# Optimization experiments

Measured on AMD Instinct MI355X. Metric: run time of the kernel, lower is better.

The kernel has to match this reference:

```python
import jax, jax.numpy as jnp
import numpy as np

HSV_BINS = 32
LBP_BINS = 256
NEG_SLOPE = 0.2
ENV_CLASSES = 4
SEASON_CLASSES = 4


def rgb_to_hsv(img):
    # img: [N, 3, H, W] in [0, 1]
    img = jnp.clip(img, 0.0, 1.0)
    r, g, b = img[:, 0], img[:, 1], img[:, 2]
    maxc = img.max(axis=1)
    minc = img.min(axis=1)
    delta = maxc - minc
    mask = delta > 1e-6
    safe = jnp.where(mask, delta, 1.0)
    hue = jnp.zeros_like(maxc)
    hue = jnp.where((maxc == r) & mask, jnp.mod((g - b) / safe, 6.0), hue)
    hue = jnp.where((maxc == g) & mask, (b - r) / safe + 2.0, hue)
    hue = jnp.where((maxc == b) & mask, (r - g) / safe + 4.0, hue)
    hue = hue / 6.0
    sat = jnp.where(maxc > 1e-6, delta / jnp.maximum(maxc, 1e-6), jnp.zeros_like(maxc))
    return jnp.stack((hue, sat, maxc), axis=1)


def hist_features(hsv):
    # torch.histc(bins=32, min=0, max=1); HSV values are all in [0,1],
    # value==1.0 falls into the last bin -> clip(floor(v*bins), 0, bins-1).
    N, C, H, W = hsv.shape
    v = hsv.reshape(N * C, H * W)
    idx = jnp.clip(jnp.floor(v * HSV_BINS).astype(jnp.int32), 0, HSV_BINS - 1)
    offset = jnp.arange(N * C, dtype=jnp.int32)[:, None] * HSV_BINS
    counts = jnp.bincount((idx + offset).reshape(-1), length=N * C * HSV_BINS)
    counts = counts.reshape(N * C, HSV_BINS).astype(jnp.float32)
    counts = counts / jnp.maximum(counts.sum(-1, keepdims=True), 1.0)
    return counts.reshape(N, C * HSV_BINS)


def lbp_features(hsv):
    N, C, H, W = hsv.shape
    p = jnp.pad(hsv, ((0, 0), (0, 0), (1, 1), (1, 1)), mode='reflect')
    offsets = [(0, 0), (0, 1), (0, 2), (1, 2), (2, 2), (2, 1), (2, 0), (1, 0)]
    codes = jnp.zeros((N, C, H, W), dtype=jnp.int32)
    for bit, (dy, dx) in enumerate(offsets):
        nb = jax.lax.dynamic_slice(p, (0, 0, dy, dx), (N, C, H, W))
        codes = codes + (nb >= hsv).astype(jnp.int32) * (1 << bit)
    codes = codes.reshape(N * C, H * W)
    offset = jnp.arange(N * C, dtype=jnp.int32)[:, None] * LBP_BINS
    counts = jnp.bincount((codes + offset).reshape(-1), length=N * C * LBP_BINS)
    counts = counts.reshape(N * C, LBP_BINS).astype(jnp.float32)
    counts = counts / jnp.maximum(counts.sum(-1, keepdims=True), 1.0)
    return counts.reshape(N, C * LBP_BINS)


def setup_inputs() -> dict:
    key = jax.random.key(0)
    k1, k2, k3, k4, k5 = jax.random.split(key, 5)
    B, T, H, W = 4, 8, 512, 512
    sequence = jax.random.uniform(k1, (B, T, 3, H, W), dtype=jnp.float32)
    high = jax.random.normal(k2, (B * T, 2048), dtype=jnp.float32)
    Wp = jax.random.normal(k3, (512, 2912), dtype=jnp.float32) * 0.02
    bp = jnp.zeros((512,), dtype=jnp.float32)
    environment_id = jax.random.randint(k4, (B,), 0, ENV_CLASSES, dtype=jnp.int64 if jax.config.jax_enable_x64 else jnp.int32)
    season_id = jax.random.randint(k5, (B,), 0, SEASON_CLASSES, dtype=jnp.int64 if jax.config.jax_enable_x64 else jnp.int32)
    return {"sequence": sequence, "high": high, "W": Wp, "b": bp,
            "environment_id": environment_id, "season_id": season_id}


def reference(sequence, high, W, b, environment_id, season_id):
    B, T, C, H, Wd = sequence.shape
    # inputs are already in [0,1) so _to_unit_rgb reduces to a clamp
    frames = jnp.clip(sequence, 0.0, 1.0).reshape(B * T, C, H, Wd)
    hsv = rgb_to_hsv(frames)                                   # [BT,3,H,W]
    low = jnp.concatenate((hist_features(hsv), lbp_features(hsv)), axis=1)  # [BT,864]
    fused = jnp.concatenate((high, low), axis=1).reshape(B, T, -1)          # [B,T,2912]
    aggregated = fused.mean(axis=1)                             # [B,2912]
    z = aggregated @ W.T + b                                    # Linear(2912->512)
    c_feat = jnp.where(z >= 0, z, NEG_SLOPE * z)                # LeakyReLU(0.2)
    env = jax.nn.one_hot(environment_id, ENV_CLASSES, dtype=jnp.float32)
    season = jax.nn.one_hot(season_id, SEASON_CLASSES, dtype=jnp.float32)
    c_cls = jnp.concatenate((env, season), axis=1)
    return (c_feat, c_cls)
```

## Files before the change

kernel.cpp:

```cpp
#include <hip/hip_runtime.h>

#define IMH 512
#define IMW 512
#define NFRAMES 32
#define HSV_BINS 32
#define LBP_BINS 256
#define FEAT_HIGH 2048
#define FEAT_LOW (3*HSV_BINS + 3*LBP_BINS)
#define FEAT_TOT (FEAT_HIGH + FEAT_LOW)
#define OUT_COLS 512
#define RSTRIP 16
#define STRIPS (IMH / RSTRIP)
#define HALVES 2
#define NHREP 16
#define NLREP 4

__device__ __forceinline__ void rgb2hsv(float r, float g, float b,
                                        float& h, float& s, float& v) {
    float maxc = fmaxf(r, fmaxf(g, b));
    float minc = fminf(r, fminf(g, b));
    float delta = maxc - minc;
    bool mask = delta > 1e-6f;
    float rd = __builtin_amdgcn_rcpf(mask ? delta : 1.0f);
    float hue = 0.0f;
    if (mask) {
        if (maxc == r) { float t = (g - b) * rd; hue = (t >= 0.0f) ? t : t + 6.0f; }
        if (maxc == g) hue = (b - r) * rd + 2.0f;
        if (maxc == b) hue = (r - g) * rd + 4.0f;
    }
    h = hue * (1.0f / 6.0f);
    s = (maxc > 1e-6f) ? delta * __builtin_amdgcn_rcpf(maxc) : 0.0f;
    v = maxc;
}

struct Row { float hl, hc, hr, sl, sc, sr, vl, vc, vr; };

__device__ __forceinline__ void cvt_shfl(const float* __restrict__ pR,
                                         const float* __restrict__ pG,
                                         const float* __restrict__ pB,
                                         int ry, int x, int lane,
                                         float r, float g, float b, Row& o) {
    rgb2hsv(r, g, b, o.hc, o.sc, o.vc);
    o.hl = __shfl(o.hc, (lane + 63) & 63);
    o.sl = __shfl(o.sc, (lane + 63) & 63);
    o.vl = __shfl(o.vc, (lane + 63) & 63);
    o.hr = __shfl(o.hc, (lane + 1) & 63);
    o.sr = __shfl(o.sc, (lane + 1) & 63);
    o.vr = __shfl(o.vc, (lane + 1) & 63);
    if (lane == 0 || lane == 63) {
        int xe = (lane == 0) ? x - 1 : x + 1;
        if (xe < 0) xe = 1;
        if (xe > IMW - 1) xe = IMW - 2;
        size_t eo = (size_t)ry * IMW + xe;
        float he, se, ve;
        rgb2hsv(pR[eo], pG[eo], pB[eo], he, se, ve);
        if (lane == 0) { o.hl = he; o.sl = se; o.vl = ve; }
        else           { o.hr = he; o.sr = se; o.vr = ve; }
    }
}

__device__ __forceinline__ void emit1(float ul, float uc, float ur,
                                      float cl, float ce, float cr,
                                      float dl, float dc, float dr,
                                      unsigned* __restrict__ hb,
                                      unsigned* __restrict__ lb) {
    int code = 0;
    code |= (ul >= ce) ? 1   : 0;
    code |= (uc >= ce) ? 2   : 0;
    code |= (ur >= ce) ? 4   : 0;
    code |= (cr >= ce) ? 8   : 0;
    code |= (dr >= ce) ? 16  : 0;
    code |= (dc >= ce) ? 32  : 0;
    code |= (dl >= ce) ? 64  : 0;
    code |= (cl >= ce) ? 128 : 0;
    int bin = min((int)(ce * 32.0f), HSV_BINS - 1);
    atomicAdd(hb + bin, 1u);
    atomicAdd(lb + code, 1u);
}

__global__ __launch_bounds__(256, 4) void hist_lbp_kernel(const float* __restrict__ seq,
                                                          unsigned* __restrict__ hist_g,
                                                          unsigned* __restrict__ lbp_g) {
    const int bid   = blockIdx.x;
    const int n     = bid >> 6;
    const int rem   = bid & 63;
    const int strip = rem >> 1;
    const int half  = rem & 1;
    const int tid   = threadIdx.x;
    const int lane  = tid & 63;
    const int w     = tid >> 6;
    const int x     = half * 256 + w * 64 + lane;
    const int yb    = strip * RSTRIP;

    __shared__ unsigned sh_hist[3][NHREP][HSV_BINS + 1];
    __shared__ unsigned sh_lbp[3][NLREP][LBP_BINS + 1];

    for (int i = tid; i < 3 * NHREP * (HSV_BINS + 1); i += 256) ((unsigned*)sh_hist)[i] = 0u;
    for (int i = tid; i < 3 * NLREP * (LBP_BINS + 1); i += 256) ((unsigned*)sh_lbp)[i] = 0u;
    __syncthreads();

    unsigned* hb0 = &sh_hist[0][lane & (NHREP - 1)][0];
    unsigned* hb1 = &sh_hist[1][lane & (NHREP - 1)][0];
    unsigned* hb2 = &sh_hist[2][lane & (NHREP - 1)][0];
    unsigned* lb0 = &sh_lbp[0][lane & (NLREP - 1)][0];
    unsigned* lb1 = &sh_lbp[1][lane & (NLREP - 1)][0];
    unsigned* lb2 = &sh_lbp[2][lane & (NLREP - 1)][0];

    const float* pR = seq + (size_t)n * 3 * IMH * IMW;
    const float* pG = pR + (size_t)IMH * IMW;
    const float* pB = pR + 2 * (size_t)IMH * IMW;

    Row U, C, D;
    const int ytop = (yb == 0) ? 1 : yb - 1;
    {
        size_t o = (size_t)ytop * IMW + x;
        cvt_shfl(pR, pG, pB, ytop, x, lane, pR[o], pG[o], pB[o], U);
        o = (size_t)yb * IMW + x;
        cvt_shfl(pR, pG, pB, yb, x, lane, pR[o], pG[o], pB[o], C);
    }
    float rn, gn, bn;
    {
        size_t o = (size_t)(yb + 1) * IMW + x;
        rn = pR[o]; gn = pG[o]; bn = pB[o];
    }

#pragma unroll 2
    for (int i = 0; i < RSTRIP; ++i) {
        int ry = yb + 1 + i;
        if (ry == IMH) ry = IMH - 2;
        cvt_shfl(pR, pG, pB, ry, x, lane, rn, gn, bn, D);
        if (i < RSTRIP - 1) {
            int r2 = yb + 2 + i;
            if (r2 == IMH) r2 = IMH - 2;
            size_t o = (size_t)r2 * IMW + x;
            rn = pR[o]; gn = pG[o]; bn = pB[o];
        }
        emit1(U.hl, U.hc, U.hr, C.hl, C.hc, C.hr, D.hl, D.hc, D.hr, hb0, lb0);
        emit1(U.sl, U.sc, U.sr, C.sl, C.sc, C.sr, D.sl, D.sc, D.sr, hb1, lb1);
        emit1(U.vl, U.vc, U.vr, C.vl, C.vc, C.vr, D.vl, D.vc, D.vr, hb2, lb2);
        U = C; C = D;
    }

    __syncthreads();
    for (int i = tid; i < 3 * HSV_BINS; i += 256) {
        int c = i >> 5, b = i & 31;
        unsigned s = 0;
#pragma unroll
        for (int r = 0; r < NHREP; ++r) s += sh_hist[c][r][b];
        if (s) atomicAdd(&hist_g[n * 3 * HSV_BINS + i], s);
    }
    for (int i = tid; i < 3 * LBP_BINS; i += 256) {
        int c = i >> 8, b = i & 255;
        unsigned s = 0;
#pragma unroll
        for (int r = 0; r < NLREP; ++r) s += sh_lbp[c][r][b];
        if (s) atomicAdd(&lbp_g[n * 3 * LBP_BINS + i], s);
    }
}

__global__ __launch_bounds__(256) void agg_cls_kernel(const float* __restrict__ high,
                                                      const unsigned* __restrict__ hist_g,
                                                      const unsigned* __restrict__ lbp_g,
                                                      const int* __restrict__ env,
                                                      const int* __restrict__ season,
                                                      float* __restrict__ agg,
                                                      float* __restrict__ out) {
    int idx = blockIdx.x * blockDim.x + threadIdx.x;
    if (idx >= 4 * FEAT_TOT + 32) return;
    if (idx >= 4 * FEAT_TOT) {
        int t = idx - 4 * FEAT_TOT;
        int i = t >> 3;
        int p = t & 7;
        float v;
        if (p < 4) v = (env[i] == p) ? 1.0f : 0.0f;
        else       v = (season[i] == p - 4) ? 1.0f : 0.0f;
        out[4 * OUT_COLS + t] = v;
        return;
    }
    int bb = idx / FEAT_TOT;
    int k  = idx % FEAT_TOT;
    float s = 0.0f;
    const float inv = 1.0f / 262144.0f;
    if (k < FEAT_HIGH) {
#pragma unroll
        for (int t = 0; t < 8; t++) s += high[(size_t)(bb * 8 + t) * FEAT_HIGH + k];
    } else if (k < FEAT_HIGH + 3 * HSV_BINS) {
        int f = k - FEAT_HIGH;
#pragma unroll
        for (int t = 0; t < 8; t++)
            s += (float)hist_g[(bb * 8 + t) * 3 * HSV_BINS + f] * inv;
    } else {
        int f = k - FEAT_HIGH - 3 * HSV_BINS;
#pragma unroll
        for (int t = 0; t < 8; t++)
            s += (float)lbp_g[(bb * 8 + t) * 3 * LBP_BINS + f] * inv;
    }
    agg[idx] = s * 0.125f;
}

__global__ __launch_bounds__(256) void gemm_kernel(const float* __restrict__ agg,
                                                   const float* __restrict__ Wm,
                                                   const float* __restrict__ bias,
                                                   float* __restrict__ out) {
    const int j = blockIdx.x;
    const int tid = threadIdx.x;
    const float* wrow = Wm + (size_t)j * FEAT_TOT;
    float a0 = 0.f, a1 = 0.f, a2 = 0.f, a3 = 0.f;
    for (int k = tid; k < FEAT_TOT; k += 256) {
        float w = wrow[k];
        a0 += agg[k] * w;
        a1 += agg[FEAT_TOT + k] * w;
        a2 += agg[2 * FEAT_TOT + k] * w;
        a3 += agg[3 * FEAT_TOT + k] * w;
    }
#pragma unroll
    for (int off = 32; off > 0; off >>= 1) {
        a0 += __shfl_down(a0, off);
        a1 += __shfl_down(a1, off);
        a2 += __shfl_down(a2, off);
        a3 += __shfl_down(a3, off);
    }
    __shared__ float red[4][4];
    if ((tid & 63) == 0) {
        int w = tid >> 6;
        red[w][0] = a0; red[w][1] = a1; red[w][2] = a2; red[w][3] = a3;
    }
    __syncthreads();
    if (tid < 4) {
        float z = red[0][tid] + red[1][tid] + red[2][tid] + red[3][tid] + bias[j];
        out[tid * OUT_COLS + j] = (z >= 0.0f) ? z : 0.2f * z;
    }
}

extern "C" void kernel_launch(void* const* d_in, const int* in_sizes, int n_in,
                              void* d_out, int out_size, void* d_ws, size_t ws_size,
                              hipStream_t stream) {
    const float* seq    = (const float*)d_in[0];
    const float* high   = (const float*)d_in[1];
    const float* Wm     = (const float*)d_in[2];
    const float* bias   = (const float*)d_in[3];
    const int*   env    = (const int*)d_in[4];
    const int*   season = (const int*)d_in[5];
    float* out = (float*)d_out;

    unsigned* hist_g = (unsigned*)d_ws;
    unsigned* lbp_g  = hist_g + NFRAMES * 3 * HSV_BINS;
    float*    agg    = (float*)(lbp_g + NFRAMES * 3 * LBP_BINS);

    size_t histBytes = (size_t)(NFRAMES * 3 * HSV_BINS + NFRAMES * 3 * LBP_BINS) * sizeof(unsigned);
    hipMemsetAsync(d_ws, 0, histBytes, stream);

    hist_lbp_kernel<<<NFRAMES * STRIPS * HALVES, 256, 0, stream>>>(seq, hist_g, lbp_g);
    agg_cls_kernel<<<(4 * FEAT_TOT + 32 + 255) / 256, 256, 0, stream>>>(high, hist_g, lbp_g, env, season, agg, out);
    gemm_kernel<<<OUT_COLS, 256, 0, stream>>>(agg, Wm, bias, out);
}
```

Before: 180.6 us.

## Process four columns per thread with float4 loads and per-wave row blocks

Remaps the histogram/LBP kernel so each thread handles four adjacent columns loaded as float4, and each wave covers a 4-row block instead of every thread walking 16 rows. This reduces the number of load instructions and cross-lane shuffles per pixel, and raises memory parallelism. In exchange, each wave recomputes HSV for two halo rows per 4-row block, adding redundant conversion work and register pressure.

```diff
diff --git a/kernel.cpp b/kernel.cpp
--- a/kernel.cpp
+++ b/kernel.cpp
@@ -9,9 +9,8 @@
 #define FEAT_LOW (3*HSV_BINS + 3*LBP_BINS)
 #define FEAT_TOT (FEAT_HIGH + FEAT_LOW)
 #define OUT_COLS 512
-#define RSTRIP 16
-#define STRIPS (IMH / RSTRIP)
-#define HALVES 2
+#define BROWS 16
+#define STRIPS (IMH / BROWS)
 #define NHREP 16
 #define NLREP 4
 
@@ -33,30 +32,41 @@
     v = maxc;
 }
 
-struct Row { float hl, hc, hr, sl, sc, sr, vl, vc, vr; };
-
-__device__ __forceinline__ void cvt_shfl(const float* __restrict__ pR,
+struct W6 { float h[6], s[6], v[6]; };
+
+__device__ __forceinline__ void cvt_row6(const float* __restrict__ pR,
                                          const float* __restrict__ pG,
                                          const float* __restrict__ pB,
-                                         int ry, int x, int lane,
-                                         float r, float g, float b, Row& o) {
-    rgb2hsv(r, g, b, o.hc, o.sc, o.vc);
-    o.hl = __shfl(o.hc, (lane + 63) & 63);
-    o.sl = __shfl(o.sc, (lane + 63) & 63);
-    o.vl = __shfl(o.vc, (lane + 63) & 63);
-    o.hr = __shfl(o.hc, (lane + 1) & 63);
-    o.sr = __shfl(o.sc, (lane + 1) & 63);
-    o.vr = __shfl(o.vc, (lane + 1) & 63);
-    if (lane == 0 || lane == 63) {
-        int xe = (lane == 0) ? x - 1 : x + 1;
-        if (xe < 0) xe = 1;
-        if (xe > IMW - 1) xe = IMW - 2;
-        size_t eo = (size_t)ry * IMW + xe;
-        float he, se, ve;
-        rgb2hsv(pR[eo], pG[eo], pB[eo], he, se, ve);
-        if (lane == 0) { o.hl = he; o.sl = se; o.vl = ve; }
-        else           { o.hr = he; o.sr = se; o.vr = ve; }
-    }
+                                         int ry, int x0, int lane,
+                                         bool edge, bool edge_right, int ecol,
+                                         bool refl_l, bool refl_r, W6& o) {
+    size_t off = (size_t)ry * IMW + x0;
+    float4 r4 = *(const float4*)(pR + off);
+    float4 g4 = *(const float4*)(pG + off);
+    float4 b4 = *(const float4*)(pB + off);
+    float er = 0.f, eg = 0.f, eb = 0.f;
+    if (edge) {
+        size_t eo = (size_t)ry * IMW + ecol;
+        er = pR[eo]; eg = pG[eo]; eb = pB[eo];
+    }
+    rgb2hsv(r4.x, g4.x, b4.x, o.h[1], o.s[1], o.v[1]);
+    rgb2hsv(r4.y, g4.y, b4.y, o.h[2], o.s[2], o.v[2]);
+    rgb2hsv(r4.z, g4.z, b4.z, o.h[3], o.s[3], o.v[3]);
+    rgb2hsv(r4.w, g4.w, b4.w, o.h[4], o.s[4], o.v[4]);
+    o.h[0] = __shfl(o.h[4], (lane + 63) & 63);
+    o.s[0] = __shfl(o.s[4], (lane + 63) & 63);
+    o.v[0] = __shfl(o.v[4], (lane + 63) & 63);
+    o.h[5] = __shfl(o.h[1], (lane + 1) & 63);
+    o.s[5] = __shfl(o.s[1], (lane + 1) & 63);
+    o.v[5] = __shfl(o.v[1], (lane + 1) & 63);
+    if (edge) {
+        float eh, es, ev;
+        rgb2hsv(er, eg, eb, eh, es, ev);
+        if (edge_right) { o.h[5] = eh; o.s[5] = es; o.v[5] = ev; }
+        else            { o.h[0] = eh; o.s[0] = es; o.v[0] = ev; }
+    }
+    if (refl_l) { o.h[0] = o.h[2]; o.s[0] = o.s[2]; o.v[0] = o.v[2]; }
+    if (refl_r) { o.h[5] = o.h[3]; o.s[5] = o.s[3]; o.v[5] = o.v[3]; }
 }
 
 __device__ __forceinline__ void emit1(float ul, float uc, float ur,
@@ -78,6 +88,14 @@
     atomicAdd(lb + code, 1u);
 }
 
+#define EMIT_SITE(U, C, D, j)                                                          \
+    emit1(U.h[j-1], U.h[j], U.h[j+1], C.h[j-1], C.h[j], C.h[j+1],                      \
+          D.h[j-1], D.h[j], D.h[j+1], hb0, lb0);                                       \
+    emit1(U.s[j-1], U.s[j], U.s[j+1], C.s[j-1], C.s[j], C.s[j+1],                      \
+          D.s[j-1], D.s[j], D.s[j+1], hb1, lb1);                                       \
+    emit1(U.v[j-1], U.v[j], U.v[j+1], C.v[j-1], C.v[j], C.v[j+1],                      \
+          D.v[j-1], D.v[j], D.v[j+1], hb2, lb2);
+
 __global__ __launch_bounds__(256, 4) void hist_lbp_kernel(const float* __restrict__ seq,
                                                           unsigned* __restrict__ hist_g,
                                                           unsigned* __restrict__ lbp_g) {
@@ -89,8 +107,14 @@
     const int tid   = threadIdx.x;
     const int lane  = tid & 63;
     const int w     = tid >> 6;
-    const int x     = half * 256 + w * 64 + lane;
-    const int yb    = strip * RSTRIP;
+    const int x0    = half * 256 + lane * 4;
+    const int gy    = strip * BROWS + w * 4;
+
+    const bool edge_right = (half == 0);
+    const bool edge   = edge_right ? (lane == 63) : (lane == 0);
+    const int  ecol   = edge_right ? (x0 + 4) : (x0 - 1);
+    const bool refl_l = (half == 0) && (lane == 0);
+    const bool refl_r = (half == 1) && (lane == 63);
 
     __shared__ unsigned sh_hist[3][NHREP][HSV_BINS + 1];
     __shared__ unsigned sh_lbp[3][NLREP][LBP_BINS + 1];
@@ -110,35 +134,20 @@
     const float* pG = pR + (size_t)IMH * IMW;
     const float* pB = pR + 2 * (size_t)IMH * IMW;
 
-    Row U, C, D;
-    const int ytop = (yb == 0) ? 1 : yb - 1;
-    {
-        size_t o = (size_t)ytop * IMW + x;
-        cvt_shfl(pR, pG, pB, ytop, x, lane, pR[o], pG[o], pB[o], U);
-        o = (size_t)yb * IMW + x;
-        cvt_shfl(pR, pG, pB, yb, x, lane, pR[o], pG[o], pB[o], C);
-    }
-    float rn, gn, bn;
-    {
-        size_t o = (size_t)(yb + 1) * IMW + x;
-        rn = pR[o]; gn = pG[o]; bn = pB[o];
-    }
-
-#pragma unroll 2
-    for (int i = 0; i < RSTRIP; ++i) {
-        int ry = yb + 1 + i;
+    W6 A, B, Cn;
+    const int ytop = (gy == 0) ? 1 : gy - 1;
+    cvt_row6(pR, pG, pB, ytop, x0, lane, edge, edge_right, ecol, refl_l, refl_r, A);
+    cvt_row6(pR, pG, pB, gy,   x0, lane, edge, edge_right, ecol, refl_l, refl_r, B);
+
+    for (int i = 0; i < 4; ++i) {
+        int ry = gy + 1 + i;
         if (ry == IMH) ry = IMH - 2;
-        cvt_shfl(pR, pG, pB, ry, x, lane, rn, gn, bn, D);
-        if (i < RSTRIP - 1) {
-            int r2 = yb + 2 + i;
-            if (r2 == IMH) r2 = IMH - 2;
-            size_t o = (size_t)r2 * IMW + x;
-            rn = pR[o]; gn = pG[o]; bn = pB[o];
-        }
-        emit1(U.hl, U.hc, U.hr, C.hl, C.hc, C.hr, D.hl, D.hc, D.hr, hb0, lb0);
-        emit1(U.sl, U.sc, U.sr, C.sl, C.sc, C.sr, D.sl, D.sc, D.sr, hb1, lb1);
-        emit1(U.vl, U.vc, U.vr, C.vl, C.vc, C.vr, D.vl, D.vc, D.vr, hb2, lb2);
-        U = C; C = D;
+        cvt_row6(pR, pG, pB, ry, x0, lane, edge, edge_right, ecol, refl_l, refl_r, Cn);
+        EMIT_SITE(A, B, Cn, 2);
+        EMIT_SITE(A, B, Cn, 3);
+        EMIT_SITE(A, B, Cn, 1);
+        EMIT_SITE(A, B, Cn, 4);
+        A = B; B = Cn;
     }
 
     __syncthreads();
@@ -250,7 +259,7 @@
     size_t histBytes = (size_t)(NFRAMES * 3 * HSV_BINS + NFRAMES * 3 * LBP_BINS) * sizeof(unsigned);
     hipMemsetAsync(d_ws, 0, histBytes, stream);
 
-    hist_lbp_kernel<<<NFRAMES * STRIPS * HALVES, 256, 0, stream>>>(seq, hist_g, lbp_g);
+    hist_lbp_kernel<<<NFRAMES * STRIPS * 2, 256, 0, stream>>>(seq, hist_g, lbp_g);
     agg_cls_kernel<<<(4 * FEAT_TOT + 32 + 255) / 256, 256, 0, stream>>>(high, hist_g, lbp_g, env, season, agg, out);
     gemm_kernel<<<OUT_COLS, 256, 0, stream>>>(agg, Wm, bias, out);
 }
```

Result: no change. 183.5 us (+1.6%).
